# Kernel optimization log

Hardware: AMD Instinct MI355X
Metric: run time of the kernel (lower is better)

Reference implementation:

```python
import jax, jax.numpy as jnp
import numpy as np
from jax import lax

L = 2        # encoder layers
D = 256      # d_model
H = 8        # nhead
DH = D // H  # head dim
CF = 2       # compression_factor (default in CustomizedAttn)
FF = 2048    # dim_feedforward
B = 10       # batch (forced: null_k has shape (10,1,D))
HH = 40
WW = 40
T = HH * WW  # seq len = 1600
EPS = 1e-5


def setup_inputs() -> dict:
    key = jax.random.key(0)
    ks = jax.random.split(key, 16)
    f = lambda k, shp: jax.random.normal(k, shp, jnp.float32) * 0.02
    return {
        "src": jax.random.normal(ks[0], (B, D, HH, WW), jnp.float32),
        "pos_embed": jax.random.normal(ks[1], (B, D, HH, WW), jnp.float32),
        "Wq": f(ks[2], (L, D, D)),
        "Wk": f(ks[3], (L, D, D)),
        "Wv": f(ks[4], (L, D, D)),
        "Wo": f(ks[5], (L, D, D)),
        "bo": jnp.zeros((L, D), jnp.float32),
        "conv_w": f(ks[6], (L, D, D // H, CF)),  # grouped Conv1d weight [out, in/groups, k]
        "conv_b": jnp.zeros((L, D), jnp.float32),
        "null_k": f(ks[7], (L, B, 1, D)),
        "null_v": f(ks[8], (L, B, 1, D)),
        "ln1_g": jnp.ones((L, D), jnp.float32),
        "ln1_b": jnp.zeros((L, D), jnp.float32),
        "ln2_g": jnp.ones((L, D), jnp.float32),
        "ln2_b": jnp.zeros((L, D), jnp.float32),
        "W1": f(ks[9], (L, FF, D)),
        "b1": jnp.zeros((L, FF), jnp.float32),
        "W2": f(ks[10], (L, D, FF)),
        "b2": jnp.zeros((L, D), jnp.float32),
    }


def _layernorm(x, g, b):
    m = jnp.mean(x, axis=-1, keepdims=True)
    v = jnp.var(x, axis=-1, keepdims=True)
    return (x - m) * lax.rsqrt(v + EPS) * g + b


def _attn(x, pos, Wq, Wk, Wv, Wo, bo, cw, cb, nk, nv):
    # x, pos: [B, T, D]
    qk = x + pos
    q = qk @ Wq.T
    k = qk @ Wk.T
    v = x @ Wv.T
    # torch: padding = cf - t % cf -> always in [1, cf], so padding ALWAYS applied
    pad = CF - (T % CF)
    k = jnp.pad(k, ((0, 0), (pad, 0), (0, 0)))
    v = jnp.pad(v, ((0, 0), (pad, 0), (0, 0)))

    def compress(t_):  # grouped strided Conv1d over time, shared weights for k and v
        y = lax.conv_general_dilated(
            t_.transpose(0, 2, 1), cw, (CF,), "VALID",
            dimension_numbers=("NCH", "OIH", "NCH"), feature_group_count=H)
        return (y + cb[None, :, None]).transpose(0, 2, 1)

    k = jnp.concatenate([nk, compress(k)], axis=1)  # [B, Tc+10, D]
    v = jnp.concatenate([nv, compress(v)], axis=1)
    split = lambda t_: t_.reshape(B, t_.shape[1], H, DH).transpose(0, 2, 1, 3)
    qh, kh, vh = split(q), split(k), split(v)
    # NOTE: scale uses FULL d_model (d ** -0.5), faithful to the source.
    dots = jnp.einsum("bhid,bhjd->bhij", qh, kh) * (D ** -0.5)
    # NOTE: the source computes softmax(dots) but then overwrites it with
    # dropout(dots); at inference attention weights are the raw scaled dots.
    out = jnp.einsum("bhij,bhjd->bhid", dots, vh)
    out = out.transpose(0, 2, 1, 3).reshape(B, T, D)
    return out @ Wo.T + bo


def reference(src, pos_embed, Wq, Wk, Wv, Wo, bo, conv_w, conv_b, null_k, null_v,
              ln1_g, ln1_b, ln2_g, ln2_b, W1, b1, W2, b2):
    x = src.reshape(B, D, T).transpose(0, 2, 1)        # [B, T, D]
    pos = pos_embed.reshape(B, D, T).transpose(0, 2, 1)
    for l in range(L):
        a = _attn(x, pos, Wq[l], Wk[l], Wv[l], Wo[l], bo[l],
                  conv_w[l], conv_b[l], null_k[l], null_v[l])
        x = _layernorm(x + a, ln1_g[l], ln1_b[l])
        ff = jnp.maximum(x @ W1[l].T + b1[l], 0.0) @ W2[l].T + b2[l]
        x = _layernorm(x + ff, ln2_g[l], ln2_b[l])
    return x.transpose(0, 2, 1).reshape(B, D, HH, WW)
```

## Files before the change

### kernel.cpp

```cpp
#include <hip/hip_runtime.h>
#include <math.h>

typedef __attribute__((ext_vector_type(8))) short short8;
typedef __attribute__((ext_vector_type(4))) short short4v;
typedef __attribute__((ext_vector_type(4))) float f32x4;
typedef unsigned int u32;

constexpr int Bsz = 10;
constexpr int Dm  = 256;
constexpr int Hh  = 8;
constexpr int Tt  = 1600;
constexpr int FFd = 2048;
constexpr int Tkv = 802;
constexpr int JCH = 8;
constexpr size_t Fsz  = (size_t)Bsz * Tt * Dm;
constexpr size_t PAD  = 65536;
constexpr size_t KVsz = (size_t)Bsz * Tkv * Dm;
constexpr size_t FHsz = (size_t)Bsz * Tt * FFd;
constexpr size_t WBsz = 2621440;

__device__ float g_x[Fsz];
__device__ float g_qk[Fsz];
__device__ float g_t[Fsz];
__device__ float g_kc[KVsz];
__device__ float g_vc[KVsz];
__device__ float g_kvm[(size_t)Bsz * Hh * 32 * 32];
__device__ float g_kvp[(size_t)JCH * Bsz * Hh * 32 * 32];
__device__ float g_pos[Fsz];
__device__ unsigned short g_xb[Fsz + PAD];
__device__ unsigned short g_qkb[Fsz + PAD];
__device__ unsigned short g_tb[Fsz + PAD];
__device__ unsigned short g_qb[Fsz + PAD];
__device__ unsigned short g_ffh[FHsz + PAD];
__device__ unsigned short g_wb[WBsz];
__device__ unsigned short g_wo2[(size_t)Bsz * Dm * Dm];

__device__ __forceinline__ float* selbuf(int id) {
  switch (id) {
    case 0: return g_x;
    case 1: return g_qk;
    case 2: return g_t;
    case 3: return g_kc;
    case 4: return g_vc;
    default: return g_kvm;
  }
}
__device__ __forceinline__ unsigned short* selbufb(int id) {
  switch (id) {
    case 0: return g_xb;
    case 1: return g_qkb;
    case 2: return g_tb;
    case 3: return g_ffh;
    default: return g_qb;
  }
}

__device__ __forceinline__ unsigned short f2b(float x) {
  unsigned int u = __float_as_uint(x);
  u += 0x7FFFu + ((u >> 16) & 1u);
  return (unsigned short)(u >> 16);
}
__device__ __forceinline__ float b2f(unsigned short u) {
  return __uint_as_float(((unsigned int)u) << 16);
}

__global__ __launch_bounds__(256) void wconv_all_k(
    const float* __restrict__ Wk, const float* __restrict__ Wq,
    const float* __restrict__ Wv, const float* __restrict__ Wo,
    const float* __restrict__ W1, const float* __restrict__ W2) {
  const int i = blockIdx.x * 256 + threadIdx.x;
  float v;
  if (i < 262144) {
    const int l = i >> 17, r = i & 131071;
    v = (r < 65536) ? Wk[l * 65536 + r] : Wq[l * 65536 + (r - 65536)];
  } else if (i < 393216) {
    v = Wv[i - 262144];
  } else if (i < 524288) {
    v = Wo[i - 393216];
  } else if (i < 1572864) {
    v = W1[i - 524288];
  } else {
    v = W2[i - 1572864];
  }
  g_wb[i] = f2b(v);
}

__global__ __launch_bounds__(256) void trans_in2_k(const float* __restrict__ src,
                                                   const float* __restrict__ pose) {
  __shared__ float ts[32][33];
  __shared__ float tp[32][33];
  const int tx = threadIdx.x & 31, ty = threadIdx.x >> 5;
  const int t0 = blockIdx.x * 32, d0 = blockIdx.y * 32, b = blockIdx.z;
  #pragma unroll
  for (int i = ty; i < 32; i += 8) {
    const size_t gi = ((size_t)(b * Dm + d0 + i)) * Tt + t0 + tx;
    ts[i][tx] = src[gi];
    tp[i][tx] = pose[gi];
  }
  __syncthreads();
  #pragma unroll
  for (int i = ty; i < 32; i += 8) {
    const size_t idx = ((size_t)(b * Tt + t0 + i)) * Dm + d0 + tx;
    const float s = ts[tx][i], p = tp[tx][i];
    g_x[idx] = s;
    g_pos[idx] = p;
    g_xb[idx] = f2b(s);
    g_qkb[idx] = f2b(s + p);
  }
}

__global__ __launch_bounds__(256) void trans_out_k(float* out) {
  __shared__ float tile[32][33];
  const int tx = threadIdx.x & 31, ty = threadIdx.x >> 5;
  const int t0 = blockIdx.x * 32, d0 = blockIdx.y * 32, b = blockIdx.z;
  #pragma unroll
  for (int i = ty; i < 32; i += 8)
    tile[i][tx] = g_x[((size_t)(b * Tt + t0 + i)) * Dm + d0 + tx];
  __syncthreads();
  #pragma unroll
  for (int i = ty; i < 32; i += 8)
    out[((size_t)(b * Dm + d0 + i)) * Tt + t0 + tx] = tile[tx][i];
}

template<int BN, bool DUAL, bool PERB, bool RELU, bool BIAS, bool CBF16>
__global__ __launch_bounds__(256) void gemm2_k(
    int Aid, int woff, const float* __restrict__ bias, int Cid, int C2id,
    int NB, int M, int N, int K) {
  constexpr int BM = 128, BK = 64;
  constexpr int ACH = BM * 8;
  constexpr int BCH = BN * 8;
  constexpr int NW = BN / 32;
  __shared__ short8 As8[3][ACH];
  __shared__ short8 Bs8[3][BCH];
  const int tid = threadIdx.x;
  const int lane = tid & 63, wid = tid >> 6;
  const int wr = wid >> 1, wc = wid & 1;

  const int nwg = gridDim.x;
  const int bid = blockIdx.x;
  const int q = nwg >> 3, r = nwg & 7;
  const int xcd = bid & 7, seq = bid >> 3;
  const int wgid = (xcd < r ? xcd * (q + 1) : r * (q + 1) + (xcd - r) * q) + seq;

  int m0, n0, mlim;
  const unsigned short* W16;
  if constexpr (PERB) {
    const int per = 13 * NB;
    const int b = wgid / per;
    const int rem = wgid - b * per;
    m0 = b * Tt + (rem / NB) * BM;
    n0 = (rem % NB) * BN;
    mlim = b * Tt + Tt;
    W16 = g_wo2 + (size_t)b * 65536;
  } else {
    m0 = (wgid / NB) * BM;
    n0 = (wgid % NB) * BN;
    mlim = M;
    W16 = g_wb + woff;
  }

  const unsigned short* A16 = selbufb(Aid);
  const bool second = DUAL && (n0 >= 256);
  float* Cf = selbuf(second ? C2id : Cid);
  unsigned short* C16 = selbufb(second ? C2id : Cid);
  const int gn0 = second ? n0 - 256 : n0;
  const int cstride = DUAL ? 256 : N;

  f32x4 acc[4][NW];
  #pragma unroll
  for (int m = 0; m < 4; ++m)
    #pragma unroll
    for (int n = 0; n < NW; ++n) acc[m][n] = (f32x4){0.f, 0.f, 0.f, 0.f};

  const int lkc = lane >> 4, lrc = lane & 15;

  auto stage = [&](int t, int buf) {
    const int k0 = t * BK;
    #pragma unroll
    for (int i = 0; i < ACH / 256; ++i) {
      const int c = tid + i * 256;
      const int row = c >> 3, kc = c & 7;
      const unsigned short* gs = A16 + (size_t)(m0 + row) * K + k0 +
                                 ((kc ^ (row & 7)) << 3);
      __builtin_amdgcn_global_load_lds(
          (const __attribute__((address_space(1))) u32*)gs,
          (__attribute__((address_space(3))) u32*)&As8[buf][c], 16, 0, 0);
    }
    #pragma unroll
    for (int i = 0; i < BCH / 256; ++i) {
      const int c = tid + i * 256;
      const int row = c >> 3, kc = c & 7;
      const unsigned short* gs = W16 + (size_t)(n0 + row) * K + k0 +
                                 ((kc ^ (row & 7)) << 3);
      __builtin_amdgcn_global_load_lds(
          (const __attribute__((address_space(1))) u32*)gs,
          (__attribute__((address_space(3))) u32*)&Bs8[buf][c], 16, 0, 0);
    }
  };

  const int nt = K / BK;
  stage(0, 0);
  if (nt > 1) stage(1, 1);
  int cur = 0, nxt = 2;
  for (int t = 0; t < nt; ++t) {
    if (t + 1 < nt) {
      asm volatile("s_waitcnt vmcnt(6)" ::: "memory");
    } else {
      asm volatile("s_waitcnt vmcnt(0)" ::: "memory");
    }
    __builtin_amdgcn_sched_barrier(0);
    __builtin_amdgcn_s_barrier();
    __builtin_amdgcn_sched_barrier(0);
    if (t + 2 < nt) stage(t + 2, nxt);
    #pragma unroll
    for (int kk = 0; kk < 2; ++kk) {
      short8 af[4], bf[NW];
      #pragma unroll
      for (int m = 0; m < 4; ++m) {
        const int r2 = wr * 64 + m * 16 + lrc;
        af[m] = As8[cur][r2 * 8 + ((kk * 4 + lkc) ^ (r2 & 7))];
      }
      #pragma unroll
      for (int n = 0; n < NW; ++n) {
        const int cn = wc * (BN / 2) + n * 16 + lrc;
        bf[n] = Bs8[cur][cn * 8 + ((kk * 4 + lkc) ^ (cn & 7))];
      }
      #pragma unroll
      for (int m = 0; m < 4; ++m)
        #pragma unroll
        for (int n = 0; n < NW; ++n)
          acc[m][n] = __builtin_amdgcn_mfma_f32_16x16x32_bf16(
              af[m], bf[n], acc[m][n], 0, 0, 0);
    }
    cur = (cur == 2) ? 0 : cur + 1;
    nxt = (nxt == 2) ? 0 : nxt + 1;
  }

  constexpr int CSTR = (BN == 64) ? BN + 4 : BN;
  float* ldsC = (float*)&As8[0][0];
  {
    asm volatile("s_waitcnt vmcnt(0)" ::: "memory");
    __builtin_amdgcn_s_barrier();
    const int r0 = lkc * 4;
    #pragma unroll
    for (int m = 0; m < 4; ++m)
      #pragma unroll
      for (int n = 0; n < NW; ++n) {
        const int col = wc * (BN / 2) + n * 16 + lrc;
        #pragma unroll
        for (int j = 0; j < 4; ++j)
          ldsC[(wr * 64 + m * 16 + r0 + j) * CSTR + col] = acc[m][n][j];
      }
    __syncthreads();
  }
  if constexpr (CBF16) {
    constexpr int CH = BM * BN / 8;
    #pragma unroll
    for (int i = 0; i < CH / 256; ++i) {
      const int c = tid + i * 256;
      const int rowl = c / (BN / 8), col8 = (c % (BN / 8)) * 8;
      if (PERB && m0 + rowl >= mlim) continue;
      short8 v;
      #pragma unroll
      for (int j = 0; j < 8; ++j) {
        float x = ldsC[rowl * CSTR + col8 + j];
        if (BIAS) x += bias[gn0 + col8 + j];
        if (RELU) x = fmaxf(x, 0.f);
        v[j] = (short)f2b(x);
      }
      *(short8*)(C16 + (size_t)(m0 + rowl) * cstride + gn0 + col8) = v;
    }
  } else {
    constexpr int CH = BM * BN / 4;
    #pragma unroll
    for (int i = 0; i < CH / 256; ++i) {
      const int c = tid + i * 256;
      const int rowl = c / (BN / 4), col4 = (c % (BN / 4)) * 4;
      if (PERB && m0 + rowl >= mlim) continue;
      float4 v;
      float* pv = &v.x;
      #pragma unroll
      for (int j = 0; j < 4; ++j) {
        float x = ldsC[rowl * CSTR + col4 + j];
        if (BIAS) x += bias[gn0 + col4 + j];
        if (RELU) x = fmaxf(x, 0.f);
        pv[j] = x;
      }
      *(float4*)(Cf + (size_t)(m0 + rowl) * cstride + gn0 + col4) = v;
    }
  }
}

__global__ __launch_bounds__(512, 1) void gemmf_k(
    int Aid, int w1off, int w2off, const float* __restrict__ b1p,
    const float* __restrict__ b2p) {
  constexpr int BM = 128, NCH = 32;
  __shared__ short8 Al[BM * 32];
  __shared__ short8 w1c[2][1024];
  __shared__ short8 w2c[2][1024];
  __shared__ short8 h8[BM * 4];
  __shared__ float b1f[1024];
  const int tid = threadIdx.x;
  const int lane = tid & 63, wid = tid >> 6;
  const int lkc = lane >> 4, lrc = lane & 15;
  const int nwg = gridDim.x, bid = blockIdx.x;
  const int q = nwg >> 3, r = nwg & 7;
  const int xcd = bid & 7, seq = bid >> 3;
  const int wgid = (xcd < r ? xcd * (q + 1) : r * (q + 1) + (xcd - r) * q) + seq;
  const int half = (wgid >= 125) ? 1 : 0;
  const int m0 = (wgid - half * 125) * BM;
  const int hb = half * 1024;
  const unsigned short* A16 = selbufb(Aid);
  const unsigned short* W1p = g_wb + w1off;
  const unsigned short* W2p = g_wb + w2off;
  float* Cf = half ? g_t : g_qk;

  #pragma unroll
  for (int i = 0; i < 8; ++i) {
    const int c = tid + i * 512;
    const int row = c >> 5, kc = c & 31;
    const unsigned short* gs = A16 + (size_t)(m0 + row) * 256 +
                               ((kc ^ (row & 31)) << 3);
    __builtin_amdgcn_global_load_lds(
        (const __attribute__((address_space(1))) u32*)gs,
        (__attribute__((address_space(3))) u32*)&Al[c], 16, 0, 0);
  }
  #pragma unroll
  for (int i = 0; i < 2; ++i) {
    const int c = tid + i * 512;
    __builtin_amdgcn_global_load_lds(
        (const __attribute__((address_space(1))) u32*)(b1p + hb + c),
        (__attribute__((address_space(3))) u32*)&b1f[c], 4, 0, 0);
  }
  auto stage_w = [&](int ch, int buf) {
    const int kb = hb + ch * 32;
    #pragma unroll
    for (int i = 0; i < 2; ++i) {
      const int c = tid + i * 512;
      const int row = c >> 5, kc = c & 31;
      const unsigned short* gs = W1p + (size_t)(kb + row) * 256 +
                                 ((kc ^ (row & 31)) << 3);
      __builtin_amdgcn_global_load_lds(
          (const __attribute__((address_space(1))) u32*)gs,
          (__attribute__((address_space(3))) u32*)&w1c[buf][c], 16, 0, 0);
    }
    #pragma unroll
    for (int i = 0; i < 2; ++i) {
      const int c = tid + i * 512;
      const int row = c >> 2, kc = c & 3;
      const int g = (kc ^ (row & 3) ^ ((row >> 2) & 3)) & 3;
      const unsigned short* gs = W2p + (size_t)row * 2048 + kb + (g << 3);
      __builtin_amdgcn_global_load_lds(
          (const __attribute__((address_space(1))) u32*)gs,
          (__attribute__((address_space(3))) u32*)&w2c[buf][c], 16, 0, 0);
    }
  };
  stage_w(0, 0);

  const int wr = wid >> 2, wc = wid & 3;
  f32x4 acc2[4][4];
  #pragma unroll
  for (int m = 0; m < 4; ++m)
    #pragma unroll
    for (int n = 0; n < 4; ++n) acc2[m][n] = (f32x4){0.f, 0.f, 0.f, 0.f};

  for (int ch = 0; ch < NCH; ++ch) {
    const int cur = ch & 1;
    if (ch) {
      __builtin_amdgcn_sched_barrier(0);
      __builtin_amdgcn_s_barrier();
      __builtin_amdgcn_sched_barrier(0);
    }
    if (ch + 1 < NCH) {
      stage_w(ch + 1, cur ^ 1);
      asm volatile("s_waitcnt vmcnt(4)" ::: "memory");
    } else {
      asm volatile("s_waitcnt vmcnt(0)" ::: "memory");
    }
    __builtin_amdgcn_sched_barrier(0);
    __builtin_amdgcn_s_barrier();
    __builtin_amdgcn_sched_barrier(0);

    f32x4 a1[2];
    a1[0] = (f32x4){0.f, 0.f, 0.f, 0.f};
    a1[1] = (f32x4){0.f, 0.f, 0.f, 0.f};
    const int r1 = wid * 16 + lrc;
    #pragma unroll
    for (int s = 0; s < 8; ++s) {
      short8 af = Al[r1 * 32 + ((s * 4 + lkc) ^ (r1 & 31))];
      #pragma unroll
      for (int n = 0; n < 2; ++n) {
        const int cn = n * 16 + lrc;
        short8 bf = w1c[cur][cn * 32 + ((s * 4 + lkc) ^ (cn & 31))];
        a1[n] = __builtin_amdgcn_mfma_f32_16x16x32_bf16(af, bf, a1[n], 0, 0, 0);
      }
    }
    unsigned short* h16 = (unsigned short*)h8;
    #pragma unroll
    for (int n = 0; n < 2; ++n) {
      const int col = n * 16 + lrc;
      const float bb = b1f[ch * 32 + col];
      #pragma unroll
      for (int j = 0; j < 4; ++j) {
        const int row = wid * 16 + lkc * 4 + j;
        float v = fmaxf(a1[n][j] + bb, 0.f);
        const int g = ((col >> 3) ^ (row & 3) ^ ((row >> 2) & 3)) & 3;
        h16[row * 32 + g * 8 + (col & 7)] = f2b(v);
      }
    }
    asm volatile("s_waitcnt lgkmcnt(0)" ::: "memory");
    __builtin_amdgcn_sched_barrier(0);
    __builtin_amdgcn_s_barrier();
    __builtin_amdgcn_sched_barrier(0);

    short8 af2[4], bf2[4];
    #pragma unroll
    for (int m = 0; m < 4; ++m) {
      const int r2 = wr * 64 + m * 16 + lrc;
      af2[m] = h8[r2 * 4 + ((lkc ^ (r2 & 3) ^ ((r2 >> 2) & 3)) & 3)];
    }
    #pragma unroll
    for (int n = 0; n < 4; ++n) {
      const int cn = wc * 64 + n * 16 + lrc;
      bf2[n] = w2c[cur][cn * 4 + ((lkc ^ (cn & 3) ^ ((cn >> 2) & 3)) & 3)];
    }
    #pragma unroll
    for (int m = 0; m < 4; ++m)
      #pragma unroll
      for (int n = 0; n < 4; ++n)
        acc2[m][n] = __builtin_amdgcn_mfma_f32_16x16x32_bf16(
            af2[m], bf2[n], acc2[m][n], 0, 0, 0);
  }

  const int r0 = lkc * 4;
  #pragma unroll
  for (int m = 0; m < 4; ++m) {
    const int gm = m0 + wr * 64 + m * 16 + r0;
    #pragma unroll
    for (int n = 0; n < 4; ++n) {
      const int gn = wc * 64 + n * 16 + lrc;
      const float bb = (half == 0) ? b2p[gn] : 0.f;
      #pragma unroll
      for (int j = 0; j < 4; ++j)
        Cf[(size_t)(gm + j) * 256 + gn] = acc2[m][n][j] + bb;
    }
  }
}

__global__ __launch_bounds__(256) void compress2_k(
    const float* __restrict__ cw, const float* __restrict__ cb,
    const float* __restrict__ nk, const float* __restrict__ nv) {
  __shared__ float rows[32][256];
  const int tc0 = 1 + blockIdx.x * 16;
  const int b = blockIdx.y;
  const int z = blockIdx.z;
  const int tid = threadIdx.x;
  const int o = tid;
  const int g = o >> 5;

  const unsigned short* srcbuf = z ? g_ffh : g_tb;
  const float* nul = z ? nv : nk;
  float* outb = (z ? g_vc : g_kc) + (size_t)b * Tkv * Dm;

  const int r0g = 2 * tc0 - 2;
  const unsigned short* src = srcbuf + ((size_t)b * Tt + r0g) * Dm;
  #pragma unroll
  for (int i = 0; i < 4; ++i) {
    const int c = tid + i * 256;
    const int row = c >> 5, off = (c & 31) * 8;
    short8 v = *(const short8*)(src + (size_t)row * 256 + off);
    #pragma unroll
    for (int j = 0; j < 8; ++j)
      rows[row][off + j] = b2f((unsigned short)v[j]);
  }

  float we[32], wo[32];
  {
    const float4* wp = (const float4*)(cw + o * 64);
    #pragma unroll
    for (int i = 0; i < 16; ++i) {
      float4 w4 = wp[i];
      we[i * 2 + 0] = w4.x; wo[i * 2 + 0] = w4.y;
      we[i * 2 + 1] = w4.z; wo[i * 2 + 1] = w4.w;
    }
  }
  const float bias = cb[o];
  if (blockIdx.x == 0) {
    outb[o] = nul[b * Dm + o];
    outb[Dm + o] = bias;
  }
  __syncthreads();

  float* outp = outb + o;
  #pragma unroll
  for (int t = 0; t < 16; ++t) {
    const int lr = 2 * t;
    const float* p0 = &rows[lr][g * 32];
    const float* p1 = &rows[lr + 1][g * 32];
    float acc = bias;
    #pragma unroll
    for (int i4 = 0; i4 < 8; ++i4) {
      float4 a0 = *(const float4*)(p0 + i4 * 4);
      float4 a1 = *(const float4*)(p1 + i4 * 4);
      acc = fmaf(we[i4 * 4 + 0], a0.x, acc);
      acc = fmaf(we[i4 * 4 + 1], a0.y, acc);
      acc = fmaf(we[i4 * 4 + 2], a0.z, acc);
      acc = fmaf(we[i4 * 4 + 3], a0.w, acc);
      acc = fmaf(wo[i4 * 4 + 0], a1.x, acc);
      acc = fmaf(wo[i4 * 4 + 1], a1.y, acc);
      acc = fmaf(wo[i4 * 4 + 2], a1.z, acc);
      acc = fmaf(wo[i4 * 4 + 3], a1.w, acc);
    }
    outp[(size_t)(1 + tc0 + t) * Dm] = acc;
  }
}

__global__ __launch_bounds__(256) void kvout1_k() {
  __shared__ float kl[8][32];
  __shared__ float vl[8][32];
  const int bh = blockIdx.x;
  const int js = blockIdx.y;
  const int b = bh >> 3, h = bh & 7;
  const int j0 = js * 101;
  const int jend = (j0 + 101 < Tkv) ? j0 + 101 : Tkv;

  const int tid = threadIdx.x;
  const int lr = tid >> 5;
  const int lc = tid & 31;
  const int e = tid >> 3;
  const int d0 = (tid & 7) * 4;

  float a0 = 0.f, a1 = 0.f, a2 = 0.f, a3 = 0.f;
  const size_t base = (size_t)b * Tkv * Dm + h * 32;

  for (int jc = j0; jc < jend; jc += 8) {
    const int jr = jc + lr;
    if (jr < jend) {
      kl[lr][lc] = g_kc[base + (size_t)jr * Dm + lc];
      vl[lr][lc] = g_vc[base + (size_t)jr * Dm + lc];
    } else {
      kl[lr][lc] = 0.f;
      vl[lr][lc] = 0.f;
    }
    __syncthreads();
    #pragma unroll
    for (int r = 0; r < 8; ++r) {
      const float kf = kl[r][e];
      const float* vr = &vl[r][d0];
      a0 = fmaf(kf, vr[0], a0);
      a1 = fmaf(kf, vr[1], a1);
      a2 = fmaf(kf, vr[2], a2);
      a3 = fmaf(kf, vr[3], a3);
    }
    __syncthreads();
  }
  float* op = g_kvp + ((size_t)js * 80 + bh) * 1024 + e * 32 + d0;
  op[0] = a0; op[1] = a1; op[2] = a2; op[3] = a3;
}

__global__ __launch_bounds__(256) void kvout2_k() {
  const int bh = blockIdx.x;
  const int tid = threadIdx.x;
  const int e = tid >> 3;
  const int d0 = (tid & 7) * 4;
  float a0 = 0.f, a1 = 0.f, a2 = 0.f, a3 = 0.f;
  #pragma unroll
  for (int s = 0; s < JCH; ++s) {
    const float* p = g_kvp + ((size_t)s * 80 + bh) * 1024 + e * 32 + d0;
    a0 += p[0]; a1 += p[1]; a2 += p[2]; a3 += p[3];
  }
  float* op = g_kvm + (size_t)bh * 1024 + e * 32 + d0;
  op[0] = a0 * 0.0625f;
  op[1] = a1 * 0.0625f;
  op[2] = a2 * 0.0625f;
  op[3] = a3 * 0.0625f;
}

__global__ __launch_bounds__(256) void wo2_k(int wooff) {
  const int n = blockIdx.x, b = blockIdx.y;
  const int he = threadIdx.x;
  const int h = he >> 5, e = he & 31;
  const float* kp = g_kvm + ((size_t)(b * Hh + h) * 32 + e) * 32;
  const unsigned short* wp = g_wb + wooff + (size_t)n * Dm + h * 32;
  float acc = 0.f;
  #pragma unroll
  for (int d = 0; d < 32; ++d) acc = fmaf(kp[d], b2f(wp[d]), acc);
  g_wo2[(size_t)b * 65536 + (size_t)n * Dm + he] = f2b(acc);
}

__global__ __launch_bounds__(256) void ln_k(int did, int did2, const float* g,
                                            const float* beta, int do_pos) {
  const int lane = threadIdx.x & 63;
  const int wave = threadIdx.x >> 6;
  const size_t row = (size_t)blockIdx.x * 4 + wave;
  float4 xv = ((const float4*)g_x)[row * 64 + lane];
  float4 dv = ((const float4*)selbuf(did))[row * 64 + lane];
  float v[4] = {xv.x + dv.x, xv.y + dv.y, xv.z + dv.z, xv.w + dv.w};
  if (did2 >= 0) {
    float4 d2 = ((const float4*)selbuf(did2))[row * 64 + lane];
    v[0] += d2.x; v[1] += d2.y; v[2] += d2.z; v[3] += d2.w;
  }
  float sum = v[0] + v[1] + v[2] + v[3];
  float sq = v[0]*v[0] + v[1]*v[1] + v[2]*v[2] + v[3]*v[3];
  #pragma unroll
  for (int off = 32; off; off >>= 1) {
    sum += __shfl_xor(sum, off);
    sq  += __shfl_xor(sq, off);
  }
  const float mean = sum * (1.f / 256.f);
  const float var = sq * (1.f / 256.f) - mean * mean;
  const float rs = rsqrtf(var + 1e-5f);
  float4 gg = ((const float4*)g)[lane];
  float4 bb = ((const float4*)beta)[lane];
  float4 ov;
  ov.x = (v[0] - mean) * rs * gg.x + bb.x;
  ov.y = (v[1] - mean) * rs * gg.y + bb.y;
  ov.z = (v[2] - mean) * rs * gg.z + bb.z;
  ov.w = (v[3] - mean) * rs * gg.w + bb.w;
  ((float4*)g_x)[row * 64 + lane] = ov;
  short4v sv;
  sv[0] = (short)f2b(ov.x); sv[1] = (short)f2b(ov.y);
  sv[2] = (short)f2b(ov.z); sv[3] = (short)f2b(ov.w);
  *(short4v*)&g_xb[(row * 64 + lane) * 4] = sv;
  if (do_pos) {
    float4 pv = ((const float4*)g_pos)[row * 64 + lane];
    short4v qv;
    qv[0] = (short)f2b(ov.x + pv.x); qv[1] = (short)f2b(ov.y + pv.y);
    qv[2] = (short)f2b(ov.z + pv.z); qv[3] = (short)f2b(ov.w + pv.w);
    *(short4v*)&g_qkb[(row * 64 + lane) * 4] = qv;
  }
}

extern "C" void kernel_launch(void* const* d_in, const int* in_sizes, int n_in,
                              void* d_out, int out_size, void* d_ws, size_t ws_size,
                              hipStream_t stream) {
  const float* src  = (const float*)d_in[0];
  const float* pose = (const float*)d_in[1];
  const float* Wq   = (const float*)d_in[2];
  const float* Wk   = (const float*)d_in[3];
  const float* Wv   = (const float*)d_in[4];
  const float* Wo   = (const float*)d_in[5];
  const float* bo   = (const float*)d_in[6];
  const float* cw   = (const float*)d_in[7];
  const float* cb   = (const float*)d_in[8];
  const float* nk   = (const float*)d_in[9];
  const float* nv   = (const float*)d_in[10];
  const float* ln1g = (const float*)d_in[11];
  const float* ln1b = (const float*)d_in[12];
  const float* ln2g = (const float*)d_in[13];
  const float* ln2b = (const float*)d_in[14];
  const float* W1   = (const float*)d_in[15];
  const float* b1   = (const float*)d_in[16];
  const float* W2   = (const float*)d_in[17];
  const float* b2   = (const float*)d_in[18];

  const int MT = Bsz * Tt;
  const dim3 tgrid(Tt / 32, Dm / 32, Bsz);

  const int OV = 262144, OO = 393216, O1 = 524288, O2 = 1572864;
  wconv_all_k<<<10240, 256, 0, stream>>>(Wk, Wq, Wv, Wo, W1, W2);
  trans_in2_k<<<tgrid, 256, 0, stream>>>(src, pose);

  const int MB = MT / 128;
  for (int l = 0; l < 2; ++l) {
    const float* bo_l = bo + (size_t)l * Dm;
    const float* cw_l = cw + (size_t)l * Dm * 64;
    const float* cb_l = cb + (size_t)l * Dm;
    const float* nk_l = nk + (size_t)l * Bsz * Dm;
    const float* nv_l = nv + (size_t)l * Bsz * Dm;
    const float* b1_l = b1 + (size_t)l * FFd;
    const float* b2_l = b2 + (size_t)l * Dm;
    const int wkq = l * 131072;
    const int wv = OV + l * 65536, wo = OO + l * 65536;
    const int w1 = O1 + l * 524288, w2 = O2 + l * 524288;

    gemm2_k<64, true, false, false, false, true><<<8 * MB, 256, 0, stream>>>(
        1, wkq, nullptr, 2, 4, 8, MT, 512, Dm);
    gemm2_k<64, false, false, false, false, true><<<4 * MB, 256, 0, stream>>>(
        0, wv, nullptr, 3, 3, 4, MT, Dm, Dm);
    compress2_k<<<dim3(50, Bsz, 2), 256, 0, stream>>>(cw_l, cb_l, nk_l, nv_l);
    kvout1_k<<<dim3(Bsz * Hh, JCH), 256, 0, stream>>>();
    kvout2_k<<<Bsz * Hh, 256, 0, stream>>>();
    wo2_k<<<dim3(Dm, Bsz), 256, 0, stream>>>(wo);
    gemm2_k<64, false, true, false, true, false><<<Bsz * 13 * 4, 256, 0, stream>>>(
        4, 0, bo_l, 2, 2, 4, MT, Dm, Dm);
    ln_k<<<MT / 4, 256, 0, stream>>>(2, -1, ln1g + l * Dm, ln1b + l * Dm, 0);

    gemmf_k<<<250, 512, 0, stream>>>(0, w1, w2, b1_l, b2_l);
    ln_k<<<MT / 4, 256, 0, stream>>>(1, 2, ln2g + l * Dm, ln2b + l * Dm,
                                     l == 0 ? 1 : 0);
  }

  trans_out_k<<<tgrid, 256, 0, stream>>>((float*)d_out);
}
```

Before: 378.7 us.

## Split fused FFN into four hidden-dim quarters with register-resident A tiles

The fused FFN kernel now divides the 2048 hidden dimension into four 512-wide slices instead of two, launching 500 blocks rather than 250. LDS is merged into a single shared buffer, the A tile is kept in registers, and launch bounds are relaxed so several blocks can reside per CU. The two extra fp32 partial outputs are written into the otherwise unused FFN-hidden buffer and summed inside the second layernorm. This aims for more parallelism and occupancy, at the cost of extra partial-sum traffic and a simpler wait-all pipeline with less load overlap.

```diff
diff --git a/kernel.cpp b/kernel.cpp
--- a/kernel.cpp
+++ b/kernel.cpp
@@ -31,7 +31,7 @@
 __device__ unsigned short g_qkb[Fsz + PAD];
 __device__ unsigned short g_tb[Fsz + PAD];
 __device__ unsigned short g_qb[Fsz + PAD];
-__device__ unsigned short g_ffh[FHsz + PAD];
+__device__ __attribute__((aligned(16))) unsigned short g_ffh[FHsz + PAD];
 __device__ unsigned short g_wb[WBsz];
 __device__ unsigned short g_wo2[(size_t)Bsz * Dm * Dm];
 
@@ -42,7 +42,9 @@
     case 2: return g_t;
     case 3: return g_kc;
     case 4: return g_vc;
-    default: return g_kvm;
+    case 5: return g_kvm;
+    case 6: return (float*)g_ffh;
+    default: return (float*)g_ffh + Fsz;
   }
 }
 __device__ __forceinline__ unsigned short* selbufb(int id) {
@@ -291,15 +293,13 @@
   }
 }
 
-__global__ __launch_bounds__(512, 1) void gemmf_k(
+__global__ __launch_bounds__(512, 4) void gemmf_k(
     int Aid, int w1off, int w2off, const float* __restrict__ b1p,
     const float* __restrict__ b2p) {
-  constexpr int BM = 128, NCH = 32;
-  __shared__ short8 Al[BM * 32];
-  __shared__ short8 w1c[2][1024];
-  __shared__ short8 w2c[2][1024];
-  __shared__ short8 h8[BM * 4];
-  __shared__ float b1f[1024];
+  constexpr int BM = 128, NCH = 16;
+  __shared__ short8 ws[4096];
+  __shared__ short8 h8[512];
+  __shared__ float b1f[512];
   const int tid = threadIdx.x;
   const int lane = tid & 63, wid = tid >> 6;
   const int lkc = lane >> 4, lrc = lane & 15;
@@ -307,13 +307,16 @@
   const int q = nwg >> 3, r = nwg & 7;
   const int xcd = bid & 7, seq = bid >> 3;
   const int wgid = (xcd < r ? xcd * (q + 1) : r * (q + 1) + (xcd - r) * q) + seq;
-  const int half = (wgid >= 125) ? 1 : 0;
-  const int m0 = (wgid - half * 125) * BM;
-  const int hb = half * 1024;
+  const int qd = wgid / 125;
+  const int m0 = (wgid - qd * 125) * BM;
+  const int hb = qd * 512;
   const unsigned short* A16 = selbufb(Aid);
   const unsigned short* W1p = g_wb + w1off;
   const unsigned short* W2p = g_wb + w2off;
-  float* Cf = half ? g_t : g_qk;
+  float* Cf;
+  if (qd == 0) Cf = g_qk;
+  else if (qd == 1) Cf = g_t;
+  else Cf = (float*)g_ffh + (size_t)(qd - 2) * Fsz;
 
   #pragma unroll
   for (int i = 0; i < 8; ++i) {
@@ -323,15 +326,28 @@
                                ((kc ^ (row & 31)) << 3);
     __builtin_amdgcn_global_load_lds(
         (const __attribute__((address_space(1))) u32*)gs,
-        (__attribute__((address_space(3))) u32*)&Al[c], 16, 0, 0);
-  }
-  #pragma unroll
-  for (int i = 0; i < 2; ++i) {
-    const int c = tid + i * 512;
-    __builtin_amdgcn_global_load_lds(
-        (const __attribute__((address_space(1))) u32*)(b1p + hb + c),
-        (__attribute__((address_space(3))) u32*)&b1f[c], 4, 0, 0);
-  }
+        (__attribute__((address_space(3))) u32*)&ws[c], 16, 0, 0);
+  }
+  __builtin_amdgcn_global_load_lds(
+      (const __attribute__((address_space(1))) u32*)(b1p + hb + tid),
+      (__attribute__((address_space(3))) u32*)&b1f[tid], 4, 0, 0);
+  asm volatile("s_waitcnt vmcnt(0)" ::: "memory");
+  __builtin_amdgcn_sched_barrier(0);
+  __builtin_amdgcn_s_barrier();
+
+  const int mg = wid >> 1, ng = wid & 1;
+  short8 areg[2][8];
+  #pragma unroll
+  for (int m = 0; m < 2; ++m)
+    #pragma unroll
+    for (int s = 0; s < 8; ++s) {
+      const int r2 = mg * 32 + m * 16 + lrc;
+      areg[m][s] = ws[r2 * 32 + ((s * 4 + lkc) ^ (r2 & 31))];
+    }
+  asm volatile("s_waitcnt lgkmcnt(0)" ::: "memory");
+  __builtin_amdgcn_sched_barrier(0);
+  __builtin_amdgcn_s_barrier();
+
   auto stage_w = [&](int ch, int buf) {
     const int kb = hb + ch * 32;
     #pragma unroll
@@ -342,7 +358,7 @@
                                  ((kc ^ (row & 31)) << 3);
       __builtin_amdgcn_global_load_lds(
           (const __attribute__((address_space(1))) u32*)gs,
-          (__attribute__((address_space(3))) u32*)&w1c[buf][c], 16, 0, 0);
+          (__attribute__((address_space(3))) u32*)&ws[buf * 2048 + c], 16, 0, 0);
     }
     #pragma unroll
     for (int i = 0; i < 2; ++i) {
@@ -352,7 +368,8 @@
       const unsigned short* gs = W2p + (size_t)row * 2048 + kb + (g << 3);
       __builtin_amdgcn_global_load_lds(
           (const __attribute__((address_space(1))) u32*)gs,
-          (__attribute__((address_space(3))) u32*)&w2c[buf][c], 16, 0, 0);
+          (__attribute__((address_space(3))) u32*)&ws[buf * 2048 + 1024 + c],
+          16, 0, 0);
     }
   };
   stage_w(0, 0);
@@ -366,48 +383,33 @@
 
   for (int ch = 0; ch < NCH; ++ch) {
     const int cur = ch & 1;
-    if (ch) {
-      __builtin_amdgcn_sched_barrier(0);
-      __builtin_amdgcn_s_barrier();
-      __builtin_amdgcn_sched_barrier(0);
-    }
-    if (ch + 1 < NCH) {
-      stage_w(ch + 1, cur ^ 1);
-      asm volatile("s_waitcnt vmcnt(4)" ::: "memory");
-    } else {
-      asm volatile("s_waitcnt vmcnt(0)" ::: "memory");
-    }
+    const int wb = cur * 2048;
+    asm volatile("s_waitcnt vmcnt(0)" ::: "memory");
     __builtin_amdgcn_sched_barrier(0);
     __builtin_amdgcn_s_barrier();
     __builtin_amdgcn_sched_barrier(0);
+    if (ch + 1 < NCH) stage_w(ch + 1, cur ^ 1);
 
     f32x4 a1[2];
     a1[0] = (f32x4){0.f, 0.f, 0.f, 0.f};
     a1[1] = (f32x4){0.f, 0.f, 0.f, 0.f};
-    const int r1 = wid * 16 + lrc;
+    const int cn1 = ng * 16 + lrc;
     #pragma unroll
     for (int s = 0; s < 8; ++s) {
-      short8 af = Al[r1 * 32 + ((s * 4 + lkc) ^ (r1 & 31))];
-      #pragma unroll
-      for (int n = 0; n < 2; ++n) {
-        const int cn = n * 16 + lrc;
-        short8 bf = w1c[cur][cn * 32 + ((s * 4 + lkc) ^ (cn & 31))];
-        a1[n] = __builtin_amdgcn_mfma_f32_16x16x32_bf16(af, bf, a1[n], 0, 0, 0);
+      short8 bf = ws[wb + cn1 * 32 + ((s * 4 + lkc) ^ cn1)];
+      a1[0] = __builtin_amdgcn_mfma_f32_16x16x32_bf16(areg[0][s], bf, a1[0], 0, 0, 0);
+      a1[1] = __builtin_amdgcn_mfma_f32_16x16x32_bf16(areg[1][s], bf, a1[1], 0, 0, 0);
+    }
+    unsigned short* h16 = (unsigned short*)h8;
+    #pragma unroll
+    for (int m = 0; m < 2; ++m)
+      #pragma unroll
+      for (int j = 0; j < 4; ++j) {
+        const int row = mg * 32 + m * 16 + lkc * 4 + j;
+        const float v = fmaxf(a1[m][j] + b1f[ch * 32 + cn1], 0.f);
+        const int g = ((cn1 >> 3) ^ (row & 3) ^ ((row >> 2) & 3)) & 3;
+        h16[row * 32 + g * 8 + (cn1 & 7)] = f2b(v);
       }
-    }
-    unsigned short* h16 = (unsigned short*)h8;
-    #pragma unroll
-    for (int n = 0; n < 2; ++n) {
-      const int col = n * 16 + lrc;
-      const float bb = b1f[ch * 32 + col];
-      #pragma unroll
-      for (int j = 0; j < 4; ++j) {
-        const int row = wid * 16 + lkc * 4 + j;
-        float v = fmaxf(a1[n][j] + bb, 0.f);
-        const int g = ((col >> 3) ^ (row & 3) ^ ((row >> 2) & 3)) & 3;
-        h16[row * 32 + g * 8 + (col & 7)] = f2b(v);
-      }
-    }
     asm volatile("s_waitcnt lgkmcnt(0)" ::: "memory");
     __builtin_amdgcn_sched_barrier(0);
     __builtin_amdgcn_s_barrier();
@@ -422,7 +424,7 @@
     #pragma unroll
     for (int n = 0; n < 4; ++n) {
       const int cn = wc * 64 + n * 16 + lrc;
-      bf2[n] = w2c[cur][cn * 4 + ((lkc ^ (cn & 3) ^ ((cn >> 2) & 3)) & 3)];
+      bf2[n] = ws[wb + 1024 + cn * 4 + ((lkc ^ (cn & 3) ^ ((cn >> 2) & 3)) & 3)];
     }
     #pragma unroll
     for (int m = 0; m < 4; ++m)
@@ -439,7 +441,7 @@
     #pragma unroll
     for (int n = 0; n < 4; ++n) {
       const int gn = wc * 64 + n * 16 + lrc;
-      const float bb = (half == 0) ? b2p[gn] : 0.f;
+      const float bb = (qd == 0) ? b2p[gn] : 0.f;
       #pragma unroll
       for (int j = 0; j < 4; ++j)
         Cf[(size_t)(gm + j) * 256 + gn] = acc2[m][n][j] + bb;
@@ -588,7 +590,8 @@
   g_wo2[(size_t)b * 65536 + (size_t)n * Dm + he] = f2b(acc);
 }
 
-__global__ __launch_bounds__(256) void ln_k(int did, int did2, const float* g,
+__global__ __launch_bounds__(256) void ln_k(int did, int did2, int did3,
+                                            int did4, const float* g,
                                             const float* beta, int do_pos) {
   const int lane = threadIdx.x & 63;
   const int wave = threadIdx.x >> 6;
@@ -599,6 +602,14 @@
   if (did2 >= 0) {
     float4 d2 = ((const float4*)selbuf(did2))[row * 64 + lane];
     v[0] += d2.x; v[1] += d2.y; v[2] += d2.z; v[3] += d2.w;
+  }
+  if (did3 >= 0) {
+    float4 d3 = ((const float4*)selbuf(did3))[row * 64 + lane];
+    v[0] += d3.x; v[1] += d3.y; v[2] += d3.z; v[3] += d3.w;
+  }
+  if (did4 >= 0) {
+    float4 d4 = ((const float4*)selbuf(did4))[row * 64 + lane];
+    v[0] += d4.x; v[1] += d4.y; v[2] += d4.z; v[3] += d4.w;
   }
   float sum = v[0] + v[1] + v[2] + v[3];
   float sq = v[0]*v[0] + v[1]*v[1] + v[2]*v[2] + v[3]*v[3];
@@ -684,10 +695,12 @@
     wo2_k<<<dim3(Dm, Bsz), 256, 0, stream>>>(wo);
     gemm2_k<64, false, true, false, true, false><<<Bsz * 13 * 4, 256, 0, stream>>>(
         4, 0, bo_l, 2, 2, 4, MT, Dm, Dm);
-    ln_k<<<MT / 4, 256, 0, stream>>>(2, -1, ln1g + l * Dm, ln1b + l * Dm, 0);
-
-    gemmf_k<<<250, 512, 0, stream>>>(0, w1, w2, b1_l, b2_l);
-    ln_k<<<MT / 4, 256, 0, stream>>>(1, 2, ln2g + l * Dm, ln2b + l * Dm,
+    ln_k<<<MT / 4, 256, 0, stream>>>(2, -1, -1, -1,
+                                     ln1g + l * Dm, ln1b + l * Dm, 0);
+
+    gemmf_k<<<500, 512, 0, stream>>>(0, w1, w2, b1_l, b2_l);
+    ln_k<<<MT / 4, 256, 0, stream>>>(1, 2, 6, 7,
+                                     ln2g + l * Dm, ln2b + l * Dm,
                                      l == 0 ? 1 : 0);
   }
 
```

After: 511.9 us. +35.2%, slower.
